# Kernel optimization log

Hardware: AMD Instinct MI355X
Metric: run time of the kernel (lower is better)

Reference implementation:

```python
import jax, jax.numpy as jnp
import numpy as np

EMBED_DIM = 512
NUM_HEADS = 8
HEAD_DIM = EMBED_DIM // NUM_HEADS
SCALE = HEAD_DIM ** -0.5


def setup_inputs() -> dict:
    key = jax.random.key(0)
    k_x, k_qkv, k_o, k_ob = jax.random.split(key, 4)
    x = jax.random.normal(k_x, (2, 2048, EMBED_DIM), dtype=jnp.float32)
    # torch Linear weight is [out, in]; we store transposed [in, out] for x @ W
    w_qkv = jax.random.normal(k_qkv, (EMBED_DIM, 3 * EMBED_DIM), dtype=jnp.float32) * (EMBED_DIM ** -0.5)
    w_o = jax.random.normal(k_o, (EMBED_DIM, EMBED_DIM), dtype=jnp.float32) * (EMBED_DIM ** -0.5)
    b_o = jax.random.normal(k_ob, (EMBED_DIM,), dtype=jnp.float32) * 0.01
    return {"x": x, "w_qkv": w_qkv, "w_o": w_o, "b_o": b_o}


def reference(x, w_qkv, w_o, b_o):
    b, s, e = x.shape
    qkv = x @ w_qkv  # [b, s, 3e]
    q, k, v = jnp.split(qkv, 3, axis=-1)
    # [b, s, e] -> [b, h, s, d]
    def heads(t):
        return t.reshape(b, s, NUM_HEADS, HEAD_DIM).transpose(0, 2, 1, 3)
    q, k, v = heads(q), heads(k), heads(v)
    scores = jnp.einsum("bhqd,bhkd->bhqk", q, k) * SCALE
    attn = jax.nn.softmax(scores, axis=-1)  # dropout = identity in eval
    out = jnp.einsum("bhqk,bhkd->bhqd", attn, v)
    out = out.transpose(0, 2, 1, 3).reshape(b, s, e)
    return out @ w_o + b_o
```

## Files before the change

### kernel.cpp

```cpp
#include <hip/hip_runtime.h>
#include <stdint.h>


typedef __bf16 bf16x8 __attribute__((ext_vector_type(8)));
typedef __bf16 bf16x4 __attribute__((ext_vector_type(4)));
typedef float f32x4 __attribute__((ext_vector_type(4)));

#define MFMA16(a, b, c) __builtin_amdgcn_mfma_f32_16x16x32_bf16((a), (b), (c), 0, 0, 0)
#define QSC 0.18033688011112042f

__device__ __forceinline__ unsigned short f2bf(float f) {
  union { float f; unsigned int u; } v;
  v.f = f;
  unsigned int u = v.u;
  u += 0x7fffu + ((u >> 16) & 1u);
  return (unsigned short)(u >> 16);
}

__device__ __forceinline__ float fast_exp2(float x) {
#if __has_builtin(__builtin_amdgcn_exp2f)
  return __builtin_amdgcn_exp2f(x);
#else
  return exp2f(x);
#endif
}

__device__ __forceinline__ void gld16(const void* g, void* lds) {
  __builtin_amdgcn_global_load_lds(
      (const __attribute__((address_space(1))) unsigned int*)g,
      (__attribute__((address_space(3))) unsigned int*)lds, 16, 0, 0);
}

__global__ void cvt_kernel(const float* __restrict__ in, unsigned short* __restrict__ out, int n4) {
  int i = blockIdx.x * blockDim.x + threadIdx.x;
  if (i < n4) {
    float4 v = ((const float4*)in)[i];
    ushort4 o;
    o.x = f2bf(v.x); o.y = f2bf(v.y); o.z = f2bf(v.z); o.w = f2bf(v.w);
    ((ushort4*)out)[i] = o;
  }
}

__global__ void tcvt_kernel(const float* __restrict__ in, unsigned short* __restrict__ out, int N) {
  __shared__ unsigned short tile[32][33];
  int tx = threadIdx.x & 31, ty = threadIdx.x >> 5;
  int n0 = blockIdx.x * 32, k0 = blockIdx.y * 32;
#pragma unroll
  for (int i = 0; i < 4; ++i)
    tile[ty + i * 8][tx] = f2bf(in[(k0 + ty + i * 8) * N + n0 + tx]);
  __syncthreads();
#pragma unroll
  for (int i = 0; i < 4; ++i)
    out[(n0 + ty + i * 8) * 512 + k0 + tx] = tile[tx][ty + i * 8];
}

__global__ __launch_bounds__(256, 2) void gemm_qkv(
    const unsigned short* __restrict__ A, const unsigned short* __restrict__ Bt,
    unsigned short* __restrict__ qws, unsigned short* __restrict__ kws,
    unsigned short* __restrict__ vtws) {
  __shared__ __align__(16) unsigned short As[128 * 64];
  __shared__ __align__(16) unsigned short Bs[128 * 64];
  const int tid = threadIdx.x;
  const int wave = tid >> 6, lane = tid & 63;
  const int quad = lane >> 4, l16 = lane & 15;
  const int waveM = (wave & 1) * 64, waveN = (wave >> 1) * 64;
  const int bm = blockIdx.x, bn = blockIdx.y;

  f32x4 acc[4][4] = {};

  const unsigned short* Ab = A + bm * 128 * 512;
  const unsigned short* Bb = Bt + bn * 128 * 512;

  for (int k0 = 0; k0 < 512; k0 += 64) {
    __syncthreads();
#pragma unroll
    for (int c = 0; c < 4; ++c) {
      int p = wave * 256 + c * 64 + lane;
      int row = p >> 3;
      int ccl = (p & 7) ^ (row & 7);
      gld16(Ab + row * 512 + k0 + ccl * 8, (char*)As + (wave * 256 + c * 64) * 16);
      gld16(Bb + row * 512 + k0 + ccl * 8, (char*)Bs + (wave * 256 + c * 64) * 16);
    }
    __syncthreads();
#pragma unroll
    for (int ks = 0; ks < 2; ++ks) {
      bf16x8 af[4], bfr[4];
#pragma unroll
      for (int mb = 0; mb < 4; ++mb) {
        int m = waveM + mb * 16 + l16;
        int cc = (ks * 4 + quad) ^ (m & 7);
        af[mb] = *(const bf16x8*)(As + m * 64 + cc * 8);
      }
#pragma unroll
      for (int nb = 0; nb < 4; ++nb) {
        int n = waveN + nb * 16 + l16;
        int cc = (ks * 4 + quad) ^ (n & 7);
        bfr[nb] = *(const bf16x8*)(Bs + n * 64 + cc * 8);
      }
#pragma unroll
      for (int mb = 0; mb < 4; ++mb)
#pragma unroll
        for (int nb = 0; nb < 4; ++nb)
          acc[mb][nb] = MFMA16(af[mb], bfr[nb], acc[mb][nb]);
    }
  }

  const int mbase = bm * 128 + waveM;
  const int nbase = bn * 128 + waveN;
  const int region = nbase >> 9;
#pragma unroll
  for (int mb = 0; mb < 4; ++mb) {
    int m0 = mbase + mb * 16 + quad * 4;
    int b = m0 >> 11, s0 = m0 & 2047;
#pragma unroll
    for (int nb = 0; nb < 4; ++nb) {
      int n = nbase + nb * 16 + l16;
      int cix = n & 511;
      int h = cix >> 6, d = cix & 63;
      int bh = b * 8 + h;
      if (region == 0) {
#pragma unroll
        for (int r = 0; r < 4; ++r)
          qws[(bh * 2048 + s0 + r) * 64 + d] = f2bf(acc[mb][nb][r] * QSC);
      } else if (region == 1) {
#pragma unroll
        for (int r = 0; r < 4; ++r)
          kws[(bh * 2048 + s0 + r) * 64 + d] = f2bf(acc[mb][nb][r]);
      } else {
        ushort4 pk;
        pk.x = f2bf(acc[mb][nb][0]);
        pk.y = f2bf(acc[mb][nb][1]);
        pk.z = f2bf(acc[mb][nb][2]);
        pk.w = f2bf(acc[mb][nb][3]);
        *(ushort4*)(vtws + (bh * 64 + d) * 2048 + s0) = pk;
      }
    }
  }
}

__global__ __launch_bounds__(256, 2) void attn_kernel(
    const unsigned short* __restrict__ qws, const unsigned short* __restrict__ kws,
    const unsigned short* __restrict__ vtws, __bf16* __restrict__ opart,
    float* __restrict__ lpart) {
  __shared__ __align__(16) unsigned short Ks[128 * 64];
  __shared__ __align__(16) unsigned short Vs[64 * 128];
  __shared__ __align__(16) __bf16 Pl[4 * 32 * 136];
  const int tid = threadIdx.x;
  const int wave = tid >> 6, lane = tid & 63;
  const int quad = lane >> 4, l16 = lane & 15;
  const int qb = blockIdx.x, bh = blockIdx.y, split = blockIdx.z;

  const unsigned short* Qb = qws + bh * 2048 * 64;
  const unsigned short* Kb = kws + bh * 2048 * 64;
  const unsigned short* Vb = vtws + bh * 64 * 2048;

  const int qbase = qb * 128 + wave * 32;
  bf16x8 qf[2][2];
#pragma unroll
  for (int s = 0; s < 2; ++s)
#pragma unroll
    for (int h = 0; h < 2; ++h)
      qf[s][h] = *(const bf16x8*)(Qb + (qbase + s * 16 + l16) * 64 + h * 32 + quad * 8);

  float l_lane[2] = {0.f, 0.f};
  f32x4 oacc[2][4] = {};
  __bf16* Pw = Pl + wave * 32 * 136;

  for (int kt = split * 8; kt < split * 8 + 8; ++kt) {
    __syncthreads();
#pragma unroll
    for (int c = 0; c < 4; ++c) {
      int p = wave * 256 + c * 64 + lane;
      {
        int row = p >> 3;
        int ccl = (p & 7) ^ (row & 7);
        gld16(Kb + (kt * 128 + row) * 64 + ccl * 8, (char*)Ks + (wave * 256 + c * 64) * 16);
      }
      {
        int row = p >> 4;
        int ccl = (p & 15) ^ (row & 15);
        gld16(Vb + row * 2048 + kt * 128 + ccl * 8, (char*)Vs + (wave * 256 + c * 64) * 16);
      }
    }
    __syncthreads();

#pragma unroll
    for (int nb = 0; nb < 8; ++nb) {
      const int krow = nb * 16 + l16;
      bf16x8 kf0 = *(const bf16x8*)(Ks + krow * 64 + (quad ^ (l16 & 7)) * 8);
      bf16x8 kf1 = *(const bf16x8*)(Ks + krow * 64 + ((4 + quad) ^ (l16 & 7)) * 8);
#pragma unroll
      for (int s = 0; s < 2; ++s) {
        f32x4 sa = {0.f, 0.f, 0.f, 0.f};
        sa = MFMA16(kf0, qf[s][0], sa);
        sa = MFMA16(kf1, qf[s][1], sa);
        float p0 = fast_exp2(sa[0]), p1 = fast_exp2(sa[1]);
        float p2 = fast_exp2(sa[2]), p3 = fast_exp2(sa[3]);
        l_lane[s] += (p0 + p1) + (p2 + p3);
        bf16x4 pk;
        pk[0] = (__bf16)p0; pk[1] = (__bf16)p1; pk[2] = (__bf16)p2; pk[3] = (__bf16)p3;
        *(bf16x4*)(Pw + (s * 16 + l16) * 136 + nb * 16 + quad * 4) = pk;
      }
    }

#pragma unroll
    for (int ks2 = 0; ks2 < 4; ++ks2) {
      bf16x8 pf0 = *(const bf16x8*)(Pw + l16 * 136 + ks2 * 32 + quad * 8);
      bf16x8 pf1 = *(const bf16x8*)(Pw + (16 + l16) * 136 + ks2 * 32 + quad * 8);
#pragma unroll
      for (int db = 0; db < 4; ++db) {
        const int vrow = db * 16 + l16;
        bf16x8 vf = *(const bf16x8*)(Vs + vrow * 128 + (((ks2 * 4 + quad) ^ l16) & 15) * 8);
        oacc[0][db] = MFMA16(pf0, vf, oacc[0][db]);
        oacc[1][db] = MFMA16(pf1, vf, oacc[1][db]);
      }
    }
  }

  const long ob = (long)(split * 16 + bh) * 2048;
#pragma unroll
  for (int s = 0; s < 2; ++s) {
#pragma unroll
    for (int db = 0; db < 4; ++db)
#pragma unroll
      for (int r = 0; r < 4; ++r) {
        int q = qbase + s * 16 + quad * 4 + r;
        opart[(ob + q) * 64 + db * 16 + l16] = (__bf16)oacc[s][db][r];
      }
    float lf = l_lane[s];
    lf += __shfl_xor(lf, 16);
    lf += __shfl_xor(lf, 32);
    if (quad == 0) lpart[ob + qbase + s * 16 + l16] = lf;
  }
}

__global__ void combine_kernel(const __bf16* __restrict__ opart, const float* __restrict__ lpart,
                               unsigned short* __restrict__ ows) {
  int idx = blockIdx.x * 256 + threadIdx.x;
  int dg = idx & 15;
  int q = (idx >> 4) & 2047;
  int bh = idx >> 15;
  bf16x4 o0 = *(const bf16x4*)(opart + ((long)bh * 2048 + q) * 64 + dg * 4);
  bf16x4 o1 = *(const bf16x4*)(opart + ((long)(16 + bh) * 2048 + q) * 64 + dg * 4);
  float inv = 1.0f / (lpart[bh * 2048 + q] + lpart[16 * 2048 + bh * 2048 + q]);
  bf16x4 o;
#pragma unroll
  for (int i = 0; i < 4; ++i) o[i] = (__bf16)(((float)o0[i] + (float)o1[i]) * inv);
  int b = bh >> 3, h = bh & 7;
  *(bf16x4*)((__bf16*)ows + ((long)(b * 2048 + q)) * 512 + h * 64 + dg * 4) = o;
}

__global__ __launch_bounds__(256, 2) void gemm_out(
    const unsigned short* __restrict__ A, const unsigned short* __restrict__ Bt,
    const float* __restrict__ bias, float* __restrict__ out) {
  __shared__ __align__(16) unsigned short As[128 * 64];
  __shared__ __align__(16) unsigned short Bs[128 * 64];
  const int tid = threadIdx.x;
  const int wave = tid >> 6, lane = tid & 63;
  const int quad = lane >> 4, l16 = lane & 15;
  const int waveM = (wave & 1) * 64, waveN = (wave >> 1) * 64;
  const int bm = blockIdx.x, bn = blockIdx.y;

  f32x4 acc[4][4] = {};

  const unsigned short* Ab = A + bm * 128 * 512;
  const unsigned short* Bb = Bt + bn * 128 * 512;

  for (int k0 = 0; k0 < 512; k0 += 64) {
    __syncthreads();
#pragma unroll
    for (int c = 0; c < 4; ++c) {
      int p = wave * 256 + c * 64 + lane;
      int row = p >> 3;
      int ccl = (p & 7) ^ (row & 7);
      gld16(Ab + row * 512 + k0 + ccl * 8, (char*)As + (wave * 256 + c * 64) * 16);
      gld16(Bb + row * 512 + k0 + ccl * 8, (char*)Bs + (wave * 256 + c * 64) * 16);
    }
    __syncthreads();
#pragma unroll
    for (int ks = 0; ks < 2; ++ks) {
      bf16x8 af[4], bfr[4];
#pragma unroll
      for (int mb = 0; mb < 4; ++mb) {
        int m = waveM + mb * 16 + l16;
        int cc = (ks * 4 + quad) ^ (m & 7);
        af[mb] = *(const bf16x8*)(As + m * 64 + cc * 8);
      }
#pragma unroll
      for (int nb = 0; nb < 4; ++nb) {
        int n = waveN + nb * 16 + l16;
        int cc = (ks * 4 + quad) ^ (n & 7);
        bfr[nb] = *(const bf16x8*)(Bs + n * 64 + cc * 8);
      }
#pragma unroll
      for (int mb = 0; mb < 4; ++mb)
#pragma unroll
        for (int nb = 0; nb < 4; ++nb)
          acc[mb][nb] = MFMA16(af[mb], bfr[nb], acc[mb][nb]);
    }
  }

  const int mbase = bm * 128 + waveM;
  const int nbase = bn * 128 + waveN;
#pragma unroll
  for (int mb = 0; mb < 4; ++mb) {
#pragma unroll
    for (int nb = 0; nb < 4; ++nb) {
      int n = nbase + nb * 16 + l16;
      float bv = bias[n];
#pragma unroll
      for (int r = 0; r < 4; ++r) {
        int m = mbase + mb * 16 + quad * 4 + r;
        out[m * 512 + n] = acc[mb][nb][r] + bv;
      }
    }
  }
}

extern "C" void kernel_launch(void* const* d_in, const int* in_sizes, int n_in,
                              void* d_out, int out_size, void* d_ws, size_t ws_size,
                              hipStream_t stream) {
  const float* x = (const float*)d_in[0];
  const float* w_qkv = (const float*)d_in[1];
  const float* w_o = (const float*)d_in[2];
  const float* b_o = (const float*)d_in[3];
  float* out = (float*)d_out;

  char* ws = (char*)d_ws;
  unsigned short* woT   = (unsigned short*)(ws + 0);
  unsigned short* qws   = (unsigned short*)(ws + 524288);
  unsigned short* kws   = (unsigned short*)(ws + 4718592);
  unsigned short* vtws  = (unsigned short*)(ws + 8912896);
  unsigned short* ows   = (unsigned short*)(ws + 13107200);
  __bf16*         opart = (__bf16*)(ws + 17301504);
  unsigned short* xb    = (unsigned short*)(ws + 17301504);
  unsigned short* wqkvT = (unsigned short*)(ws + 21495808);
  float*          lpart = (float*)(ws + 25690112);

  cvt_kernel<<<2048, 256, 0, stream>>>(x, xb, 524288);
  tcvt_kernel<<<dim3(48, 16), 256, 0, stream>>>(w_qkv, wqkvT, 1536);
  tcvt_kernel<<<dim3(16, 16), 256, 0, stream>>>(w_o, woT, 512);
  gemm_qkv<<<dim3(32, 12), 256, 0, stream>>>(xb, wqkvT, qws, kws, vtws);
  attn_kernel<<<dim3(16, 16, 2), 256, 0, stream>>>(qws, kws, vtws, opart, lpart);
  combine_kernel<<<2048, 256, 0, stream>>>(opart, lpart, ows);
  gemm_out<<<dim3(32, 4), 256, 0, stream>>>(ows, woT, b_o, out);
}
```

Measured before the change: 124.7 us.

## Fuse prep kernels, keep P in registers, split attention four ways, shrink out tile

Merges the three conversion launches into one prep kernel. In attention, K rows are loaded into LDS in a permuted order so the exponentiated score MFMA outputs can be packed directly into PV operand registers. This removes the P round-trip through LDS and cuts LDS use to allow four blocks per CU. The key split grows from 2 to 4, which makes the combine kernel sum four partials, and gemm_out uses 64-row tiles to launch more blocks. In exchange there are more partial-output writes and more combine traffic, and opart overlapping later workspace regions required moving lpart.

```diff
diff --git a/kernel.cpp b/kernel.cpp
--- a/kernel.cpp
+++ b/kernel.cpp
@@ -31,20 +31,31 @@
       (__attribute__((address_space(3))) unsigned int*)lds, 16, 0, 0);
 }
 
-__global__ void cvt_kernel(const float* __restrict__ in, unsigned short* __restrict__ out, int n4) {
-  int i = blockIdx.x * blockDim.x + threadIdx.x;
-  if (i < n4) {
-    float4 v = ((const float4*)in)[i];
+__global__ void prep_kernel(const float* __restrict__ x, const float* __restrict__ w_qkv,
+                            const float* __restrict__ w_o, unsigned short* __restrict__ xb,
+                            unsigned short* __restrict__ wqkvT, unsigned short* __restrict__ woT) {
+  __shared__ unsigned short tile[32][33];
+  int bid = blockIdx.x;
+  if (bid < 2048) {
+    int i = bid * 256 + threadIdx.x;
+    float4 v = ((const float4*)x)[i];
     ushort4 o;
     o.x = f2bf(v.x); o.y = f2bf(v.y); o.z = f2bf(v.z); o.w = f2bf(v.w);
-    ((ushort4*)out)[i] = o;
-  }
-}
-
-__global__ void tcvt_kernel(const float* __restrict__ in, unsigned short* __restrict__ out, int N) {
-  __shared__ unsigned short tile[32][33];
+    ((ushort4*)xb)[i] = o;
+    return;
+  }
+  const float* in;
+  unsigned short* out;
+  int N, bx, by;
+  if (bid < 2816) {
+    int id = bid - 2048;
+    bx = id % 48; by = id / 48; N = 1536; in = w_qkv; out = wqkvT;
+  } else {
+    int id = bid - 2816;
+    bx = id % 16; by = id / 16; N = 512; in = w_o; out = woT;
+  }
   int tx = threadIdx.x & 31, ty = threadIdx.x >> 5;
-  int n0 = blockIdx.x * 32, k0 = blockIdx.y * 32;
+  int n0 = bx * 32, k0 = by * 32;
 #pragma unroll
   for (int i = 0; i < 4; ++i)
     tile[ty + i * 8][tx] = f2bf(in[(k0 + ty + i * 8) * N + n0 + tx]);
@@ -138,13 +149,12 @@
   }
 }
 
-__global__ __launch_bounds__(256, 2) void attn_kernel(
+__global__ __launch_bounds__(256, 4) void attn_kernel(
     const unsigned short* __restrict__ qws, const unsigned short* __restrict__ kws,
     const unsigned short* __restrict__ vtws, __bf16* __restrict__ opart,
     float* __restrict__ lpart) {
   __shared__ __align__(16) unsigned short Ks[128 * 64];
   __shared__ __align__(16) unsigned short Vs[64 * 128];
-  __shared__ __align__(16) __bf16 Pl[4 * 32 * 136];
   const int tid = threadIdx.x;
   const int wave = tid >> 6, lane = tid & 63;
   const int quad = lane >> 4, l16 = lane & 15;
@@ -162,57 +172,57 @@
     for (int h = 0; h < 2; ++h)
       qf[s][h] = *(const bf16x8*)(Qb + (qbase + s * 16 + l16) * 64 + h * 32 + quad * 8);
 
+  int kgo[4], vgo[4];
+#pragma unroll
+  for (int c = 0; c < 4; ++c) {
+    int p = wave * 256 + c * 64 + lane;
+    int pos = p >> 3, cs = p & 7;
+    int key = (pos & 96) | ((pos & 12) << 1) | ((pos & 16) >> 2) | (pos & 3);
+    kgo[c] = key * 64 + (cs ^ (pos & 7)) * 8;
+    int vr = p >> 4;
+    vgo[c] = vr * 2048 + ((p & 15) ^ (vr & 15)) * 8;
+  }
+
   float l_lane[2] = {0.f, 0.f};
   f32x4 oacc[2][4] = {};
-  __bf16* Pw = Pl + wave * 32 * 136;
-
-  for (int kt = split * 8; kt < split * 8 + 8; ++kt) {
+
+  for (int kt = split * 4; kt < split * 4 + 4; ++kt) {
     __syncthreads();
 #pragma unroll
     for (int c = 0; c < 4; ++c) {
-      int p = wave * 256 + c * 64 + lane;
-      {
-        int row = p >> 3;
-        int ccl = (p & 7) ^ (row & 7);
-        gld16(Kb + (kt * 128 + row) * 64 + ccl * 8, (char*)Ks + (wave * 256 + c * 64) * 16);
-      }
-      {
-        int row = p >> 4;
-        int ccl = (p & 15) ^ (row & 15);
-        gld16(Vb + row * 2048 + kt * 128 + ccl * 8, (char*)Vs + (wave * 256 + c * 64) * 16);
-      }
-    }
-    __syncthreads();
-
-#pragma unroll
-    for (int nb = 0; nb < 8; ++nb) {
-      const int krow = nb * 16 + l16;
-      bf16x8 kf0 = *(const bf16x8*)(Ks + krow * 64 + (quad ^ (l16 & 7)) * 8);
-      bf16x8 kf1 = *(const bf16x8*)(Ks + krow * 64 + ((4 + quad) ^ (l16 & 7)) * 8);
-#pragma unroll
-      for (int s = 0; s < 2; ++s) {
-        f32x4 sa = {0.f, 0.f, 0.f, 0.f};
-        sa = MFMA16(kf0, qf[s][0], sa);
-        sa = MFMA16(kf1, qf[s][1], sa);
-        float p0 = fast_exp2(sa[0]), p1 = fast_exp2(sa[1]);
-        float p2 = fast_exp2(sa[2]), p3 = fast_exp2(sa[3]);
-        l_lane[s] += (p0 + p1) + (p2 + p3);
-        bf16x4 pk;
-        pk[0] = (__bf16)p0; pk[1] = (__bf16)p1; pk[2] = (__bf16)p2; pk[3] = (__bf16)p3;
-        *(bf16x4*)(Pw + (s * 16 + l16) * 136 + nb * 16 + quad * 4) = pk;
-      }
-    }
-
-#pragma unroll
-    for (int ks2 = 0; ks2 < 4; ++ks2) {
-      bf16x8 pf0 = *(const bf16x8*)(Pw + l16 * 136 + ks2 * 32 + quad * 8);
-      bf16x8 pf1 = *(const bf16x8*)(Pw + (16 + l16) * 136 + ks2 * 32 + quad * 8);
+      gld16(Kb + kt * 8192 + kgo[c], (char*)Ks + (wave * 256 + c * 64) * 16);
+      gld16(Vb + kt * 128 + vgo[c], (char*)Vs + (wave * 256 + c * 64) * 16);
+    }
+    __syncthreads();
+
+#pragma unroll
+    for (int c = 0; c < 4; ++c) {
+      bf16x8 af[2];
+#pragma unroll
+      for (int t = 0; t < 2; ++t) {
+        const unsigned short* kr = Ks + (c * 32 + t * 16 + l16) * 64;
+        bf16x8 kf0 = *(const bf16x8*)(kr + (quad ^ (l16 & 7)) * 8);
+        bf16x8 kf1 = *(const bf16x8*)(kr + ((4 + quad) ^ (l16 & 7)) * 8);
+#pragma unroll
+        for (int s = 0; s < 2; ++s) {
+          f32x4 sa = {0.f, 0.f, 0.f, 0.f};
+          sa = MFMA16(kf0, qf[s][0], sa);
+          sa = MFMA16(kf1, qf[s][1], sa);
+          float e0 = fast_exp2(sa[0]), e1 = fast_exp2(sa[1]);
+          float e2 = fast_exp2(sa[2]), e3 = fast_exp2(sa[3]);
+          l_lane[s] += (e0 + e1) + (e2 + e3);
+          af[s][t * 4 + 0] = (__bf16)e0;
+          af[s][t * 4 + 1] = (__bf16)e1;
+          af[s][t * 4 + 2] = (__bf16)e2;
+          af[s][t * 4 + 3] = (__bf16)e3;
+        }
+      }
 #pragma unroll
       for (int db = 0; db < 4; ++db) {
-        const int vrow = db * 16 + l16;
-        bf16x8 vf = *(const bf16x8*)(Vs + vrow * 128 + (((ks2 * 4 + quad) ^ l16) & 15) * 8);
-        oacc[0][db] = MFMA16(pf0, vf, oacc[0][db]);
-        oacc[1][db] = MFMA16(pf1, vf, oacc[1][db]);
+        const int vr = db * 16 + l16;
+        bf16x8 vf = *(const bf16x8*)(Vs + vr * 128 + (((c * 4 + quad) ^ l16) & 15) * 8);
+        oacc[0][db] = MFMA16(af[0], vf, oacc[0][db]);
+        oacc[1][db] = MFMA16(af[1], vf, oacc[1][db]);
       }
     }
   }
@@ -240,48 +250,59 @@
   int dg = idx & 15;
   int q = (idx >> 4) & 2047;
   int bh = idx >> 15;
-  bf16x4 o0 = *(const bf16x4*)(opart + ((long)bh * 2048 + q) * 64 + dg * 4);
-  bf16x4 o1 = *(const bf16x4*)(opart + ((long)(16 + bh) * 2048 + q) * 64 + dg * 4);
-  float inv = 1.0f / (lpart[bh * 2048 + q] + lpart[16 * 2048 + bh * 2048 + q]);
-  bf16x4 o;
-#pragma unroll
-  for (int i = 0; i < 4; ++i) o[i] = (__bf16)(((float)o0[i] + (float)o1[i]) * inv);
+  float a0 = 0.f, a1 = 0.f, a2 = 0.f, a3 = 0.f, lsum = 0.f;
+#pragma unroll
+  for (int s = 0; s < 4; ++s) {
+    bf16x4 o = *(const bf16x4*)(opart + ((long)(s * 16 + bh) * 2048 + q) * 64 + dg * 4);
+    a0 += (float)o[0]; a1 += (float)o[1]; a2 += (float)o[2]; a3 += (float)o[3];
+    lsum += lpart[(s * 16 + bh) * 2048 + q];
+  }
+  float inv = 1.0f / lsum;
+  bf16x4 r;
+  r[0] = (__bf16)(a0 * inv); r[1] = (__bf16)(a1 * inv);
+  r[2] = (__bf16)(a2 * inv); r[3] = (__bf16)(a3 * inv);
   int b = bh >> 3, h = bh & 7;
-  *(bf16x4*)((__bf16*)ows + ((long)(b * 2048 + q)) * 512 + h * 64 + dg * 4) = o;
+  *(bf16x4*)((__bf16*)ows + ((long)(b * 2048 + q)) * 512 + h * 64 + dg * 4) = r;
 }
 
 __global__ __launch_bounds__(256, 2) void gemm_out(
     const unsigned short* __restrict__ A, const unsigned short* __restrict__ Bt,
     const float* __restrict__ bias, float* __restrict__ out) {
-  __shared__ __align__(16) unsigned short As[128 * 64];
+  __shared__ __align__(16) unsigned short As[64 * 64];
   __shared__ __align__(16) unsigned short Bs[128 * 64];
   const int tid = threadIdx.x;
   const int wave = tid >> 6, lane = tid & 63;
   const int quad = lane >> 4, l16 = lane & 15;
-  const int waveM = (wave & 1) * 64, waveN = (wave >> 1) * 64;
+  const int waveM = (wave & 1) * 32, waveN = (wave >> 1) * 64;
   const int bm = blockIdx.x, bn = blockIdx.y;
 
-  f32x4 acc[4][4] = {};
-
-  const unsigned short* Ab = A + bm * 128 * 512;
+  f32x4 acc[2][4] = {};
+
+  const unsigned short* Ab = A + bm * 64 * 512;
   const unsigned short* Bb = Bt + bn * 128 * 512;
 
   for (int k0 = 0; k0 < 512; k0 += 64) {
     __syncthreads();
+#pragma unroll
+    for (int c = 0; c < 2; ++c) {
+      int p = wave * 128 + c * 64 + lane;
+      int row = p >> 3;
+      int ccl = (p & 7) ^ (row & 7);
+      gld16(Ab + row * 512 + k0 + ccl * 8, (char*)As + (wave * 128 + c * 64) * 16);
+    }
 #pragma unroll
     for (int c = 0; c < 4; ++c) {
       int p = wave * 256 + c * 64 + lane;
       int row = p >> 3;
       int ccl = (p & 7) ^ (row & 7);
-      gld16(Ab + row * 512 + k0 + ccl * 8, (char*)As + (wave * 256 + c * 64) * 16);
       gld16(Bb + row * 512 + k0 + ccl * 8, (char*)Bs + (wave * 256 + c * 64) * 16);
     }
     __syncthreads();
 #pragma unroll
     for (int ks = 0; ks < 2; ++ks) {
-      bf16x8 af[4], bfr[4];
-#pragma unroll
-      for (int mb = 0; mb < 4; ++mb) {
+      bf16x8 af[2], bfr[4];
+#pragma unroll
+      for (int mb = 0; mb < 2; ++mb) {
         int m = waveM + mb * 16 + l16;
         int cc = (ks * 4 + quad) ^ (m & 7);
         af[mb] = *(const bf16x8*)(As + m * 64 + cc * 8);
@@ -293,17 +314,17 @@
         bfr[nb] = *(const bf16x8*)(Bs + n * 64 + cc * 8);
       }
 #pragma unroll
-      for (int mb = 0; mb < 4; ++mb)
+      for (int mb = 0; mb < 2; ++mb)
 #pragma unroll
         for (int nb = 0; nb < 4; ++nb)
           acc[mb][nb] = MFMA16(af[mb], bfr[nb], acc[mb][nb]);
     }
   }
 
-  const int mbase = bm * 128 + waveM;
+  const int mbase = bm * 64 + waveM;
   const int nbase = bn * 128 + waveN;
 #pragma unroll
-  for (int mb = 0; mb < 4; ++mb) {
+  for (int mb = 0; mb < 2; ++mb) {
 #pragma unroll
     for (int nb = 0; nb < 4; ++nb) {
       int n = nbase + nb * 16 + l16;
@@ -335,13 +356,11 @@
   __bf16*         opart = (__bf16*)(ws + 17301504);
   unsigned short* xb    = (unsigned short*)(ws + 17301504);
   unsigned short* wqkvT = (unsigned short*)(ws + 21495808);
-  float*          lpart = (float*)(ws + 25690112);
-
-  cvt_kernel<<<2048, 256, 0, stream>>>(x, xb, 524288);
-  tcvt_kernel<<<dim3(48, 16), 256, 0, stream>>>(w_qkv, wqkvT, 1536);
-  tcvt_kernel<<<dim3(16, 16), 256, 0, stream>>>(w_o, woT, 512);
+  float*          lpart = (float*)(ws + 34078720);
+
+  prep_kernel<<<3072, 256, 0, stream>>>(x, w_qkv, w_o, xb, wqkvT, woT);
   gemm_qkv<<<dim3(32, 12), 256, 0, stream>>>(xb, wqkvT, qws, kws, vtws);
-  attn_kernel<<<dim3(16, 16, 2), 256, 0, stream>>>(qws, kws, vtws, opart, lpart);
+  attn_kernel<<<dim3(16, 16, 4), 256, 0, stream>>>(qws, kws, vtws, opart, lpart);
   combine_kernel<<<2048, 256, 0, stream>>>(opart, lpart, ows);
-  gemm_out<<<dim3(32, 4), 256, 0, stream>>>(ows, woT, b_o, out);
-}
+  gemm_out<<<dim3(64, 4), 256, 0, stream>>>(ows, woT, b_o, out);
+}
```

Result: slower. 139.7 us (+12.0%).
